# Kernel tuning notes

Hardware: AMD Instinct MI355X
Metric: run time of the kernel (lower is better)

## Reference

```python
import jax, jax.numpy as jnp
import numpy as np
from jax import lax

B, N, C = 16, 64, 256  # batch, token_num (conv channels), embedding_dim (x == c required)
MLP_HID = 12           # dim=3, expansion_factor=4

def _gaussian_kernel(size=3, mean=0.0, std=1.0):
    # Normal(mean,std).log_prob(arange(size))
    i = jnp.arange(size, dtype=jnp.float32)
    vals = -0.5 * ((i - mean) / std) ** 2 - jnp.log(std * jnp.sqrt(2.0 * jnp.pi))
    grid = jnp.exp(vals[:, None] + vals[None, :])
    return grid / grid.sum()

def setup_inputs() -> dict:
    key = jax.random.key(0)
    ks = jax.random.split(key, 8)
    inp = {
        'image_embedding': jax.random.normal(ks[0], (B, N, C), jnp.float32),
        'tmp_embedding': jax.random.normal(ks[1], (B, N, C), jnp.float32),
        'prompt_embedding1': jax.random.normal(ks[2], (B, N, C), jnp.float32),
        'prompt_embedding2': jax.random.normal(ks[3], (B, N, C), jnp.float32),
        # PromptMLP: Linear(3,12) -> GELU -> Linear(12,1)
        'mlp_w1': jax.random.normal(ks[4], (3, MLP_HID), jnp.float32) / jnp.sqrt(3.0),
        'mlp_b1': jnp.zeros((MLP_HID,), jnp.float32),
        'mlp_w2': jax.random.normal(ks[5], (MLP_HID, 1), jnp.float32) / jnp.sqrt(float(MLP_HID)),
        'mlp_b2': jnp.zeros((1,), jnp.float32),
        # GaussianConv2d learnable 3x3 kernel (shared across channels) + bias (out_channels=1)
        'gauss_w': _gaussian_kernel(3, 0.0, 1.0),
        'gauss_b': jnp.zeros((1,), jnp.float32),
    }
    return inp

def reference(image_embedding, tmp_embedding, prompt_embedding1, prompt_embedding2,
              mlp_w1, mlp_b1, mlp_w2, mlp_b2, gauss_w, gauss_b):
    b, n, c = tmp_embedding.shape
    # PromptMixer: stack (q,k,v) on last axis -> (b,n,c,3), tiny MLP to scalar
    qkv = jnp.stack([tmp_embedding, prompt_embedding1, prompt_embedding2], axis=-1)
    h = jax.nn.gelu(qkv @ mlp_w1 + mlp_b1, approximate=False)  # torch nn.GELU is exact
    etpp = (h @ mlp_w2 + mlp_b2)[..., 0]                       # (b,n,c)
    # outer product: (b,n,c) x (b,n,x) -> (b,n,c,x)
    att_m = jnp.einsum('bnc,bnx->bncx', etpp, image_embedding)
    # GaussianConv2d: weight (1, n, 3, 3) = shared 3x3 kernel repeated over in_channels=n
    w = jnp.broadcast_to(gauss_w[None, None, :, :], (1, n, 3, 3))
    att_m = lax.conv_general_dilated(att_m, w, (1, 1), [(1, 1), (1, 1)],
                                     dimension_numbers=('NCHW', 'OIHW', 'NCHW'))
    att_m = att_m + gauss_b[None, :, None, None]               # (b,1,c,x)
    s = tmp_embedding + prompt_embedding1 + prompt_embedding2  # (b,n,c)
    etq = jnp.einsum('bnx,bnc->bnxc', image_embedding, s)      # (b,n,x,c)
    # broadcasted batched matmul: (b,1,c,x) @ (b,n,x,c) -> (b,n,c,c); elementwise max (x==c)
    m = jnp.einsum('bcx,bnxd->bncd', att_m[:, 0], etq)
    att = jnp.maximum(m, etq)
    res = jnp.einsum('bncd,bnd->bnc', att, s)
    return (image_embedding, res)
```

## Files before the change

kernel.cpp:

```cpp
#include <hip/hip_runtime.h>
#include <math.h>

#define BB 16
#define NN 64
#define CC 256

__device__ __forceinline__ float gelu_exact(float x) {
    return 0.5f * x * (1.0f + erff(x * 0.70710678118654752440f));
}

__global__ void k1_mlp_reduce(const float* __restrict__ img,
                              const float* __restrict__ tmp,
                              const float* __restrict__ p1,
                              const float* __restrict__ p2,
                              const float* __restrict__ w1,
                              const float* __restrict__ b1,
                              const float* __restrict__ w2,
                              const float* __restrict__ b2,
                              float* __restrict__ etpp,
                              float* __restrict__ Spos,
                              float* __restrict__ Sneg,
                              float* __restrict__ out0) {
    int bn = blockIdx.x;
    int c  = threadIdx.x;
    int idx = bn * CC + c;
    float t  = tmp[idx];
    float q1 = p1[idx];
    float q2 = p2[idx];
    float g  = img[idx];
    out0[idx] = g;

    float acc = b2[0];
    #pragma unroll
    for (int j = 0; j < 12; ++j) {
        float h = t * w1[j] + q1 * w1[12 + j] + q2 * w1[24 + j] + b1[j];
        acc += gelu_exact(h) * w2[j];
    }
    etpp[idx] = acc;

    float s  = t + q1 + q2;
    float s2 = s * s;
    float sp = (s >= 0.0f) ? s2 : 0.0f;
    float sn = (s < 0.0f)  ? s2 : 0.0f;

    #pragma unroll
    for (int off = 32; off > 0; off >>= 1) {
        sp += __shfl_down(sp, off);
        sn += __shfl_down(sn, off);
    }
    __shared__ float swp[4], swn[4];
    int lane = threadIdx.x & 63;
    int wv   = threadIdx.x >> 6;
    if (lane == 0) { swp[wv] = sp; swn[wv] = sn; }
    __syncthreads();
    if (threadIdx.x == 0) {
        Spos[bn] = swp[0] + swp[1] + swp[2] + swp[3];
        Sneg[bn] = swn[0] + swn[1] + swn[2] + swn[3];
    }
}

__global__ void k2_gemm_M(const float* __restrict__ etpp,
                          const float* __restrict__ img,
                          float* __restrict__ M) {
    int b  = blockIdx.z;
    int c0 = blockIdx.y * 16;
    int x0 = blockIdx.x * 16;
    __shared__ float le[64][16];
    __shared__ float li[64][16];
    int tid = threadIdx.x;
    const float* eb = etpp + b * NN * CC;
    const float* ib = img  + b * NN * CC;
    #pragma unroll
    for (int k = 0; k < 4; ++k) {
        int idx = tid + k * 256;
        int n  = idx >> 4;
        int cl = idx & 15;
        le[n][cl] = eb[n * CC + c0 + cl];
        li[n][cl] = ib[n * CC + x0 + cl];
    }
    __syncthreads();
    int tx = tid & 15, ty = tid >> 4;
    float acc = 0.0f;
    #pragma unroll
    for (int n = 0; n < 64; ++n) acc += le[n][ty] * li[n][tx];
    M[b * CC * CC + (c0 + ty) * CC + x0 + tx] = acc;
}

__global__ void k3_conv(const float* __restrict__ M,
                        const float* __restrict__ gw,
                        const float* __restrict__ gb,
                        float* __restrict__ A) {
    int gid = blockIdx.x * blockDim.x + threadIdx.x;
    int x = gid & 255;
    int c = (gid >> 8) & 255;
    int b = gid >> 16;
    const float* Mb = M + b * CC * CC;
    float acc = gb[0];
    #pragma unroll
    for (int dc = 0; dc < 3; ++dc) {
        int cc = c + dc - 1;
        if (cc < 0 || cc > 255) continue;
        #pragma unroll
        for (int dx = 0; dx < 3; ++dx) {
            int xx = x + dx - 1;
            if (xx < 0 || xx > 255) continue;
            acc += gw[dc * 3 + dx] * Mb[cc * 256 + xx];
        }
    }
    A[gid] = acc;
}

__global__ void k4_P_res(const float* __restrict__ A,
                         const float* __restrict__ img,
                         const float* __restrict__ Spos,
                         const float* __restrict__ Sneg,
                         float* __restrict__ out1) {
    int b  = blockIdx.z;
    int n0 = blockIdx.y * 16;
    int c0 = blockIdx.x * 16;
    __shared__ float li[16][65];
    __shared__ float la[16][65];
    int tid = threadIdx.x;
    const float* ib = img + b * NN * CC;
    const float* Ab = A   + b * CC * CC;
    int tx = tid & 15, ty = tid >> 4;
    float acc = 0.0f;
    for (int xc = 0; xc < 256; xc += 64) {
        #pragma unroll
        for (int k = 0; k < 4; ++k) {
            int idx = tid + k * 256;
            int r  = idx >> 6;
            int xl = idx & 63;
            li[r][xl] = ib[(n0 + r) * CC + xc + xl];
            la[r][xl] = Ab[(c0 + r) * CC + xc + xl];
        }
        __syncthreads();
        #pragma unroll
        for (int x = 0; x < 64; ++x) acc += li[ty][x] * la[tx][x];
        __syncthreads();
    }
    int n = n0 + ty, c = c0 + tx;
    int idx = b * NN * CC + n * CC + c;
    float g  = ib[n * CC + c];
    float sp = Spos[b * NN + n];
    float sn = Sneg[b * NN + n];
    out1[idx] = fmaxf(acc, g) * sp + fminf(acc, g) * sn;
}

extern "C" void kernel_launch(void* const* d_in, const int* in_sizes, int n_in,
                              void* d_out, int out_size, void* d_ws, size_t ws_size,
                              hipStream_t stream) {
    const float* img = (const float*)d_in[0];
    const float* tmp = (const float*)d_in[1];
    const float* p1  = (const float*)d_in[2];
    const float* p2  = (const float*)d_in[3];
    const float* w1  = (const float*)d_in[4];
    const float* b1  = (const float*)d_in[5];
    const float* w2  = (const float*)d_in[6];
    const float* b2  = (const float*)d_in[7];
    const float* gw  = (const float*)d_in[8];
    const float* gb  = (const float*)d_in[9];

    float* out0 = (float*)d_out;
    float* out1 = out0 + BB * NN * CC;

    float* ws   = (float*)d_ws;
    float* etpp = ws;
    float* Spos = etpp + BB * NN * CC;
    float* Sneg = Spos + BB * NN;
    float* M    = Sneg + BB * NN;
    float* A    = M + BB * CC * CC;

    k1_mlp_reduce<<<BB * NN, 256, 0, stream>>>(img, tmp, p1, p2, w1, b1, w2, b2,
                                               etpp, Spos, Sneg, out0);
    k2_gemm_M<<<dim3(16, 16, 16), 256, 0, stream>>>(etpp, img, M);
    k3_conv<<<4096, 256, 0, stream>>>(M, gw, gb, A);
    k4_P_res<<<dim3(16, 4, 16), 256, 0, stream>>>(A, img, Spos, Sneg, out1);
}
```

Baseline: 41.83 us.

## Fuse conv into final GEMM, register-tile M GEMM, vectorize MLP kernel

The 3x3 Gaussian conv is merged into the final contraction kernel: each block loads a haloed tile of M into shared memory, computes the conv tile on the fly and uses it directly in a 2x2 register-tiled GEMM, so the intermediate A buffer is never written or read and one launch disappears. The M GEMM moves from 16x16 tiles with one output per thread to 64x64 tiles with 4x4 register blocking and vector loads and stores. The MLP/reduce kernel now processes four elements per thread with float4 accesses and reduces per wavefront without shared memory. In exchange, the fused kernel launches only 256 blocks and redoes halo loads, which may lower occupancy and latency hiding.

Result: no change. 42.48 us (+1.6%).

```diff
diff --git a/kernel.cpp b/kernel.cpp
--- a/kernel.cpp
+++ b/kernel.cpp
@@ -4,6 +4,8 @@
 #define BB 16
 #define NN 64
 #define CC 256
+
+typedef __attribute__((ext_vector_type(4))) float f32x4;
 
 __device__ __forceinline__ float gelu_exact(float x) {
     return 0.5f * x * (1.0f + erff(x * 0.70710678118654752440f));
@@ -21,130 +23,169 @@
                               float* __restrict__ Spos,
                               float* __restrict__ Sneg,
                               float* __restrict__ out0) {
-    int bn = blockIdx.x;
-    int c  = threadIdx.x;
-    int idx = bn * CC + c;
-    float t  = tmp[idx];
-    float q1 = p1[idx];
-    float q2 = p2[idx];
-    float g  = img[idx];
-    out0[idx] = g;
-
-    float acc = b2[0];
-    #pragma unroll
-    for (int j = 0; j < 12; ++j) {
-        float h = t * w1[j] + q1 * w1[12 + j] + q2 * w1[24 + j] + b1[j];
-        acc += gelu_exact(h) * w2[j];
-    }
-    etpp[idx] = acc;
-
-    float s  = t + q1 + q2;
-    float s2 = s * s;
-    float sp = (s >= 0.0f) ? s2 : 0.0f;
-    float sn = (s < 0.0f)  ? s2 : 0.0f;
+    int t    = threadIdx.x;
+    int bn   = blockIdx.x * 4 + (t >> 6);
+    int lane = t & 63;
+    int base = bn * CC + lane * 4;
+
+    f32x4 tv = *(const f32x4*)(tmp + base);
+    f32x4 q1 = *(const f32x4*)(p1 + base);
+    f32x4 q2 = *(const f32x4*)(p2 + base);
+    f32x4 gv = *(const f32x4*)(img + base);
+    *(f32x4*)(out0 + base) = gv;
+
+    float bb2 = b2[0];
+    f32x4 e;
+    float sp = 0.0f, sn = 0.0f;
+    #pragma unroll
+    for (int u = 0; u < 4; ++u) {
+        float acc = bb2;
+        #pragma unroll
+        for (int j = 0; j < 12; ++j) {
+            float h = tv[u] * w1[j] + q1[u] * w1[12 + j] + q2[u] * w1[24 + j] + b1[j];
+            acc += gelu_exact(h) * w2[j];
+        }
+        e[u] = acc;
+        float s  = tv[u] + q1[u] + q2[u];
+        float s2 = s * s;
+        if (s >= 0.0f) sp += s2; else sn += s2;
+    }
+    *(f32x4*)(etpp + base) = e;
 
     #pragma unroll
     for (int off = 32; off > 0; off >>= 1) {
         sp += __shfl_down(sp, off);
         sn += __shfl_down(sn, off);
     }
-    __shared__ float swp[4], swn[4];
-    int lane = threadIdx.x & 63;
-    int wv   = threadIdx.x >> 6;
-    if (lane == 0) { swp[wv] = sp; swn[wv] = sn; }
-    __syncthreads();
-    if (threadIdx.x == 0) {
-        Spos[bn] = swp[0] + swp[1] + swp[2] + swp[3];
-        Sneg[bn] = swn[0] + swn[1] + swn[2] + swn[3];
-    }
+    if (lane == 0) { Spos[bn] = sp; Sneg[bn] = sn; }
 }
 
 __global__ void k2_gemm_M(const float* __restrict__ etpp,
                           const float* __restrict__ img,
                           float* __restrict__ M) {
+    __shared__ float es[64][68];
+    __shared__ float is_[64][68];
     int b  = blockIdx.z;
-    int c0 = blockIdx.y * 16;
-    int x0 = blockIdx.x * 16;
-    __shared__ float le[64][16];
-    __shared__ float li[64][16];
-    int tid = threadIdx.x;
+    int c0 = blockIdx.y * 64;
+    int x0 = blockIdx.x * 64;
+    int t  = threadIdx.x;
     const float* eb = etpp + b * NN * CC;
     const float* ib = img  + b * NN * CC;
+
     #pragma unroll
     for (int k = 0; k < 4; ++k) {
-        int idx = tid + k * 256;
-        int n  = idx >> 4;
-        int cl = idx & 15;
-        le[n][cl] = eb[n * CC + c0 + cl];
-        li[n][cl] = ib[n * CC + x0 + cl];
+        int idx = t + k * 256;
+        int n   = idx >> 4;
+        int j   = (idx & 15) * 4;
+        *(f32x4*)&es[n][j]  = *(const f32x4*)(eb + n * CC + c0 + j);
+        *(f32x4*)&is_[n][j] = *(const f32x4*)(ib + n * CC + x0 + j);
     }
     __syncthreads();
-    int tx = tid & 15, ty = tid >> 4;
-    float acc = 0.0f;
-    #pragma unroll
-    for (int n = 0; n < 64; ++n) acc += le[n][ty] * li[n][tx];
-    M[b * CC * CC + (c0 + ty) * CC + x0 + tx] = acc;
-}
-
-__global__ void k3_conv(const float* __restrict__ M,
-                        const float* __restrict__ gw,
-                        const float* __restrict__ gb,
-                        float* __restrict__ A) {
-    int gid = blockIdx.x * blockDim.x + threadIdx.x;
-    int x = gid & 255;
-    int c = (gid >> 8) & 255;
-    int b = gid >> 16;
-    const float* Mb = M + b * CC * CC;
-    float acc = gb[0];
-    #pragma unroll
-    for (int dc = 0; dc < 3; ++dc) {
-        int cc = c + dc - 1;
-        if (cc < 0 || cc > 255) continue;
-        #pragma unroll
-        for (int dx = 0; dx < 3; ++dx) {
-            int xx = x + dx - 1;
-            if (xx < 0 || xx > 255) continue;
-            acc += gw[dc * 3 + dx] * Mb[cc * 256 + xx];
-        }
-    }
-    A[gid] = acc;
-}
-
-__global__ void k4_P_res(const float* __restrict__ A,
-                         const float* __restrict__ img,
-                         const float* __restrict__ Spos,
-                         const float* __restrict__ Sneg,
-                         float* __restrict__ out1) {
-    int b  = blockIdx.z;
-    int n0 = blockIdx.y * 16;
+
+    int tx = t & 15, ty = t >> 4;
+    float acc[4][4] = {};
+    #pragma unroll 8
+    for (int n = 0; n < 64; ++n) {
+        f32x4 ev = *(const f32x4*)&es[n][ty * 4];
+        f32x4 iv = *(const f32x4*)&is_[n][tx * 4];
+        #pragma unroll
+        for (int i = 0; i < 4; ++i)
+            #pragma unroll
+            for (int j = 0; j < 4; ++j)
+                acc[i][j] += ev[i] * iv[j];
+    }
+
+    float* Mb = M + b * CC * CC;
+    #pragma unroll
+    for (int i = 0; i < 4; ++i) {
+        f32x4 v;
+        #pragma unroll
+        for (int j = 0; j < 4; ++j) v[j] = acc[i][j];
+        *(f32x4*)(Mb + (c0 + ty * 4 + i) * CC + x0 + tx * 4) = v;
+    }
+}
+
+__global__ void k34_conv_P_res(const float* __restrict__ M,
+                               const float* __restrict__ img,
+                               const float* __restrict__ gw,
+                               const float* __restrict__ gb,
+                               const float* __restrict__ Spos,
+                               const float* __restrict__ Sneg,
+                               float* __restrict__ out1) {
+    __shared__ float Ms[18][68];
+    __shared__ float As[16][68];
+    __shared__ float gs[64][68];
+    int b  = blockIdx.y;
     int c0 = blockIdx.x * 16;
-    __shared__ float li[16][65];
-    __shared__ float la[16][65];
-    int tid = threadIdx.x;
+    int t  = threadIdx.x;
+    const float* Mb = M   + b * CC * CC;
     const float* ib = img + b * NN * CC;
-    const float* Ab = A   + b * CC * CC;
-    int tx = tid & 15, ty = tid >> 4;
-    float acc = 0.0f;
-    for (int xc = 0; xc < 256; xc += 64) {
+
+    float w[9];
+    #pragma unroll
+    for (int q = 0; q < 9; ++q) w[q] = gw[q];
+    float bias = gb[0];
+
+    int tx = t & 7;
+    int ty = t >> 3;
+    float acc[2][2] = {};
+
+    for (int x0 = 0; x0 < 256; x0 += 64) {
+        for (int idx = t; idx < 18 * 66; idx += 256) {
+            int r = idx / 66, cl = idx - r * 66;
+            int gr = c0 - 1 + r, gc = x0 - 1 + cl;
+            float v = 0.0f;
+            if (gr >= 0 && gr < 256 && gc >= 0 && gc < 256) v = Mb[gr * 256 + gc];
+            Ms[r][cl] = v;
+        }
         #pragma unroll
         for (int k = 0; k < 4; ++k) {
-            int idx = tid + k * 256;
-            int r  = idx >> 6;
-            int xl = idx & 63;
-            li[r][xl] = ib[(n0 + r) * CC + xc + xl];
-            la[r][xl] = Ab[(c0 + r) * CC + xc + xl];
+            int idx = t + k * 256;
+            int n = idx >> 4, j = (idx & 15) * 4;
+            *(f32x4*)&gs[n][j] = *(const f32x4*)(ib + n * CC + x0 + j);
         }
         __syncthreads();
         #pragma unroll
-        for (int x = 0; x < 64; ++x) acc += li[ty][x] * la[tx][x];
+        for (int k = 0; k < 4; ++k) {
+            int idx = t + k * 256;
+            int ci = idx >> 6, xi = idx & 63;
+            float a = bias;
+            #pragma unroll
+            for (int dc = 0; dc < 3; ++dc)
+                #pragma unroll
+                for (int dx = 0; dx < 3; ++dx)
+                    a += w[dc * 3 + dx] * Ms[ci + dc][xi + dx];
+            As[ci][xi] = a;
+        }
         __syncthreads();
-    }
-    int n = n0 + ty, c = c0 + tx;
-    int idx = b * NN * CC + n * CC + c;
-    float g  = ib[n * CC + c];
-    float sp = Spos[b * NN + n];
-    float sn = Sneg[b * NN + n];
-    out1[idx] = fmaxf(acc, g) * sp + fminf(acc, g) * sn;
+        #pragma unroll 4
+        for (int kk = 0; kk < 16; ++kk) {
+            f32x4 g0 = *(const f32x4*)&gs[2 * ty][kk * 4];
+            f32x4 g1 = *(const f32x4*)&gs[2 * ty + 1][kk * 4];
+            f32x4 a0 = *(const f32x4*)&As[2 * tx][kk * 4];
+            f32x4 a1 = *(const f32x4*)&As[2 * tx + 1][kk * 4];
+            #pragma unroll
+            for (int v = 0; v < 4; ++v) {
+                acc[0][0] += g0[v] * a0[v];
+                acc[0][1] += g0[v] * a1[v];
+                acc[1][0] += g1[v] * a0[v];
+                acc[1][1] += g1[v] * a1[v];
+            }
+        }
+        __syncthreads();
+    }
+
+    int n0 = 2 * ty;
+    float sp0 = Spos[b * NN + n0],     sn0 = Sneg[b * NN + n0];
+    float sp1 = Spos[b * NN + n0 + 1], sn1 = Sneg[b * NN + n0 + 1];
+    #pragma unroll
+    for (int j = 0; j < 2; ++j) {
+        int c = c0 + 2 * tx + j;
+        float g0 = ib[n0 * CC + c];
+        float g1 = ib[(n0 + 1) * CC + c];
+        out1[(b * NN + n0) * CC + c]     = fmaxf(acc[0][j], g0) * sp0 + fminf(acc[0][j], g0) * sn0;
+        out1[(b * NN + n0 + 1) * CC + c] = fmaxf(acc[1][j], g1) * sp1 + fminf(acc[1][j], g1) * sn1;
+    }
 }
 
 extern "C" void kernel_launch(void* const* d_in, const int* in_sizes, int n_in,
@@ -169,11 +210,9 @@
     float* Spos = etpp + BB * NN * CC;
     float* Sneg = Spos + BB * NN;
     float* M    = Sneg + BB * NN;
-    float* A    = M + BB * CC * CC;
-
-    k1_mlp_reduce<<<BB * NN, 256, 0, stream>>>(img, tmp, p1, p2, w1, b1, w2, b2,
-                                               etpp, Spos, Sneg, out0);
-    k2_gemm_M<<<dim3(16, 16, 16), 256, 0, stream>>>(etpp, img, M);
-    k3_conv<<<4096, 256, 0, stream>>>(M, gw, gb, A);
-    k4_P_res<<<dim3(16, 4, 16), 256, 0, stream>>>(A, img, Spos, Sneg, out1);
-}
+
+    k1_mlp_reduce<<<256, 256, 0, stream>>>(img, tmp, p1, p2, w1, b1, w2, b2,
+                                           etpp, Spos, Sneg, out0);
+    k2_gemm_M<<<dim3(4, 4, 16), 256, 0, stream>>>(etpp, img, M);
+    k34_conv_P_res<<<dim3(16, 16), 256, 0, stream>>>(M, img, gw, gb, Spos, Sneg, out1);
+}
```
